# Performance work log

Measured on AMD Instinct MI355X. Metric: run time of the kernel, lower is better.

Reference implementation:

```python
import jax, jax.numpy as jnp
import numpy as np

NUM_INPUT = 700
NUM_HIDDEN = 256
NUM_OUTPUT = 20
WIN = 50
BATCH = 512
DELAYS = (0, 16, 32)
MAX_D = 32
N_LAYERS = 2
THRESH = 0.3
ALPHA = 0.8  # membrane decay tau_m
LENS = 0.5   # surrogate-gradient window

@jax.custom_vjp
def spike_fn(u):
    # Heaviside with rectangular surrogate gradient (ActFun in the torch repo)
    return (u > 0.0).astype(u.dtype)

def _spike_fwd(u):
    return spike_fn(u), u

def _spike_bwd(u, g):
    return (g * (jnp.abs(u) < LENS).astype(u.dtype),)

spike_fn.defvjp(_spike_fwd, _spike_bwd)


def setup_inputs() -> dict:
    key = jax.random.key(0)
    ks = jax.random.split(key, 6)
    def init(k, shape, fan_in):
        return (jax.random.normal(k, shape, jnp.float32) / np.sqrt(fan_in)).astype(jnp.float32)
    return {
        "x":  jax.random.uniform(ks[0], (BATCH, WIN, NUM_INPUT), jnp.float32),
        # one input Linear per delay: [n_delays, H, In]
        "Wd": init(ks[1], (len(DELAYS), NUM_HIDDEN, NUM_INPUT), NUM_INPUT),
        "bd": jnp.zeros((len(DELAYS), NUM_HIDDEN), jnp.float32),
        # per-layer feedforward and recurrent weights
        "Wf": init(ks[2], (N_LAYERS, NUM_HIDDEN, NUM_HIDDEN), NUM_HIDDEN),
        "bf": jnp.zeros((N_LAYERS, NUM_HIDDEN), jnp.float32),
        "Wr": init(ks[3], (N_LAYERS, NUM_HIDDEN, NUM_HIDDEN), NUM_HIDDEN),
        # readout
        "Wo": init(ks[4], (NUM_OUTPUT, NUM_HIDDEN), NUM_HIDDEN),
        "bo": jnp.zeros((NUM_OUTPUT,), jnp.float32),
    }


def _forward(x, Wd, bd, Wf, bf, Wr, Wo, bo):
    B, win, _ = x.shape
    # extended_input: zeros for the first MAX_D steps, then the input
    ext = jnp.pad(x, ((0, 0), (MAX_D, 0), (0, 0)))
    # Precompute summed delayed input currents for all timesteps at once.
    cur = jnp.zeros((B, win, NUM_HIDDEN), x.dtype)
    for i, d in enumerate(DELAYS):
        sl = jax.lax.dynamic_slice_in_dim(ext, MAX_D - d, win, axis=1)
        cur = cur + jnp.einsum('bti,hi->bth', sl, Wd[i]) + bd[i]

    def step(carry, cur_t):
        mems, spks, o_mem, o_spk, o_sum, out_mot = carry
        prev = cur_t  # [B, H] summed delayed-input activations
        new_m, new_s = [], []
        for l in range(N_LAYERS):
            m = mems[l] * ALPHA * (1.0 - spks[l]) + prev @ Wf[l].T + bf[l] + spks[l] @ Wr[l].T
            s = spike_fn(m - THRESH)
            new_m.append(m)
            new_s.append(s)
            prev = s
        o_mem = o_mem * ALPHA * (1.0 - o_spk) + prev @ Wo.T + bo
        o_spk = spike_fn(o_mem - THRESH)
        o_sum = o_sum + o_spk
        out_mot = out_mot + jax.nn.softmax(o_mem, axis=1)
        return (jnp.stack(new_m), jnp.stack(new_s), o_mem, o_spk, o_sum, out_mot), None

    z = jnp.zeros((B, NUM_OUTPUT), x.dtype)
    zh = jnp.zeros((N_LAYERS, B, NUM_HIDDEN), x.dtype)
    carry0 = (zh, zh, z, z, z, z)
    carry, _ = jax.lax.scan(step, carry0, jnp.swapaxes(cur, 0, 1))
    _, _, _, _, o_sum, out_mot = carry
    return (o_sum / win, out_mot)


def reference(x, Wd, bd, Wf, bf, Wr, Wo, bo):
    return _forward(x, Wd, bd, Wf, bf, Wr, Wo, bo)
```

## Files before the change

### kernel.cpp

```cpp
#include <hip/hip_runtime.h>
#include <cstddef>

#define CUR_ELEMS (25600 * 256)
#define WROWS 65792

__global__ __launch_bounds__(256) void k0_transpose(
    const float* __restrict__ Wf, const float* __restrict__ Wr,
    const float* __restrict__ Wo, float* __restrict__ ws) {
  int tid = blockIdx.x * blockDim.x + threadIdx.x;
  float* Wr0T = ws + CUR_ELEMS;
  float* Wf1T = Wr0T + WROWS;
  float* Wr1T = Wf1T + WROWS;
  float* WoT  = Wr1T + WROWS;
  if (tid < WROWS) {
    int k = tid >> 8, h = tid & 255;
    Wr0T[tid] = (k < 256) ? Wr[h * 256 + k] : 0.f;
  } else if (tid < 2 * WROWS) {
    int i = tid - WROWS; int k = i >> 8, h = i & 255;
    Wf1T[i] = (k < 256) ? Wf[65536 + h * 256 + k] : 0.f;
  } else if (tid < 3 * WROWS) {
    int i = tid - 2 * WROWS; int k = i >> 8, h = i & 255;
    Wr1T[i] = (k < 256) ? Wr[65536 + h * 256 + k] : 0.f;
  } else if (tid < 3 * WROWS + 5140) {
    int i = tid - 3 * WROWS; int k = i / 20, j = i - k * 20;
    WoT[i] = (k < 256) ? Wo[j * 256 + k] : 0.f;
  }
}

__global__ __launch_bounds__(256) void k1_cur(
    const float* __restrict__ x, const float* __restrict__ Wd,
    const float* __restrict__ bd, float* __restrict__ cur) {
  __shared__ float As[16][132];
  __shared__ float Bs[16][132];
  const int t  = 49 - blockIdx.y;
  const int bt = blockIdx.x >> 1, ht = blockIdx.x & 1;
  const int b0 = bt * 128, h0 = ht * 128;
  const int tid = threadIdx.x;
  const int tx = tid & 15, ty = tid >> 4;
  const int r = tid & 127, half = tid >> 7;

  float acc[8][8];
#pragma unroll
  for (int i = 0; i < 8; ++i)
#pragma unroll
    for (int j = 0; j < 8; ++j) acc[i][j] = 0.f;

  const int DEL[3] = {0, 16, 32};
#pragma unroll 1
  for (int di = 0; di < 3; ++di) {
    const int d = DEL[di];
    if (t < d) continue;
    const int tsrc = t - d;
    const float* Arow = x + ((size_t)(b0 + r) * 50 + tsrc) * 700;
    const float* Brow = Wd + (size_t)di * 179200 + (size_t)(h0 + r) * 700;
#pragma unroll 1
    for (int k0 = 0; k0 < 700; k0 += 16) {
#pragma unroll
      for (int e = 0; e < 2; ++e) {
        const int kk0 = half * 8 + e * 4;
        float4 av, bv;
        if (k0 + kk0 + 3 < 700) {
          av = *(const float4*)(Arow + k0 + kk0);
          bv = *(const float4*)(Brow + k0 + kk0);
        } else {
          av = make_float4(0.f, 0.f, 0.f, 0.f);
          bv = make_float4(0.f, 0.f, 0.f, 0.f);
        }
        As[kk0 + 0][r] = av.x; As[kk0 + 1][r] = av.y;
        As[kk0 + 2][r] = av.z; As[kk0 + 3][r] = av.w;
        Bs[kk0 + 0][r] = bv.x; Bs[kk0 + 1][r] = bv.y;
        Bs[kk0 + 2][r] = bv.z; Bs[kk0 + 3][r] = bv.w;
      }
      __syncthreads();
#pragma unroll
      for (int kk = 0; kk < 16; ++kk) {
        const float4 a0 = *(const float4*)&As[kk][ty * 4];
        const float4 a1 = *(const float4*)&As[kk][64 + ty * 4];
        const float4 c0 = *(const float4*)&Bs[kk][tx * 4];
        const float4 c1 = *(const float4*)&Bs[kk][64 + tx * 4];
        const float ar[8] = {a0.x, a0.y, a0.z, a0.w, a1.x, a1.y, a1.z, a1.w};
        const float br[8] = {c0.x, c0.y, c0.z, c0.w, c1.x, c1.y, c1.z, c1.w};
#pragma unroll
        for (int rr = 0; rr < 8; ++rr)
#pragma unroll
          for (int cc = 0; cc < 8; ++cc) acc[rr][cc] += ar[rr] * br[cc];
      }
      __syncthreads();
    }
  }
  float bias[8];
#pragma unroll
  for (int q = 0; q < 2; ++q)
#pragma unroll
    for (int c = 0; c < 4; ++c) {
      const int col = h0 + q * 64 + tx * 4 + c;
      bias[q * 4 + c] = bd[col] + bd[256 + col] + bd[512 + col];
    }
#pragma unroll
  for (int p = 0; p < 2; ++p)
#pragma unroll
    for (int rr = 0; rr < 4; ++rr) {
      const int row = b0 + p * 64 + ty * 4 + rr;
      float* dst = cur + ((size_t)t * 512 + row) * 256 + h0;
      const int ai = p * 4 + rr;
      float4 v0 = make_float4(acc[ai][0] + bias[0], acc[ai][1] + bias[1],
                              acc[ai][2] + bias[2], acc[ai][3] + bias[3]);
      float4 v1 = make_float4(acc[ai][4] + bias[4], acc[ai][5] + bias[5],
                              acc[ai][6] + bias[6], acc[ai][7] + bias[7]);
      *(float4*)(dst + tx * 4) = v0;
      *(float4*)(dst + 64 + tx * 4) = v1;
    }
}

__global__ __launch_bounds__(256) void k1b_ff0(
    const float* __restrict__ Wf, const float* __restrict__ bf,
    float* __restrict__ cur) {
  __shared__ float As[16][68];
  __shared__ float Bs[16][260];
  const int m0 = blockIdx.x * 64;
  const int tid = threadIdx.x;
  const int tx = tid & 15, ty = tid >> 4;
  const int lr = tid & 63, akk = (tid >> 6) * 4;

  float acc[4][16];
#pragma unroll
  for (int i = 0; i < 4; ++i)
#pragma unroll
    for (int j = 0; j < 16; ++j) acc[i][j] = 0.f;

#pragma unroll 1
  for (int k0 = 0; k0 < 256; k0 += 16) {
    float4 av = *(const float4*)(cur + (size_t)(m0 + lr) * 256 + k0 + akk);
    As[akk + 0][lr] = av.x; As[akk + 1][lr] = av.y;
    As[akk + 2][lr] = av.z; As[akk + 3][lr] = av.w;
#pragma unroll
    for (int e = 0; e < 4; ++e) {
      const int hh = e * 64 + lr;
      float4 bv = *(const float4*)(Wf + (size_t)hh * 256 + k0 + akk);
      Bs[akk + 0][hh] = bv.x; Bs[akk + 1][hh] = bv.y;
      Bs[akk + 2][hh] = bv.z; Bs[akk + 3][hh] = bv.w;
    }
    __syncthreads();
#pragma unroll
    for (int kk = 0; kk < 16; ++kk) {
      const float4 a = *(const float4*)&As[kk][ty * 4];
      const float ar[4] = {a.x, a.y, a.z, a.w};
#pragma unroll
      for (int q = 0; q < 4; ++q) {
        const float4 bq = *(const float4*)&Bs[kk][q * 64 + tx * 4];
        const float br[4] = {bq.x, bq.y, bq.z, bq.w};
#pragma unroll
        for (int rr = 0; rr < 4; ++rr)
#pragma unroll
          for (int cc = 0; cc < 4; ++cc)
            acc[rr][q * 4 + cc] += ar[rr] * br[cc];
      }
    }
    __syncthreads();
  }
  float bias[16];
#pragma unroll
  for (int q = 0; q < 4; ++q)
#pragma unroll
    for (int c = 0; c < 4; ++c) bias[q * 4 + c] = bf[q * 64 + tx * 4 + c];
#pragma unroll
  for (int rr = 0; rr < 4; ++rr) {
    float* dst = cur + (size_t)(m0 + ty * 4 + rr) * 256;
#pragma unroll
    for (int q = 0; q < 4; ++q) {
      float4 v = make_float4(acc[rr][q * 4 + 0] + bias[q * 4 + 0],
                             acc[rr][q * 4 + 1] + bias[q * 4 + 1],
                             acc[rr][q * 4 + 2] + bias[q * 4 + 2],
                             acc[rr][q * 4 + 3] + bias[q * 4 + 3]);
      *(float4*)(dst + q * 64 + tx * 4) = v;
    }
  }
}

__device__ __forceinline__ float sum16v(const float* w) {
  float s0 = 0.f, s1 = 0.f, s2 = 0.f, s3 = 0.f;
#pragma unroll
  for (int u = 0; u < 16; u += 4) {
    s0 += w[u]; s1 += w[u + 1]; s2 += w[u + 2]; s3 += w[u + 3];
  }
  return (s0 + s1) + (s2 + s3);
}

__device__ __forceinline__ void fetch16(
    const float* __restrict__ baseA, const int* LA_, int nA_,
    const float* __restrict__ baseB, const int* LB_, int g16, int h, float* w) {
  const float* base = (g16 < nA_) ? baseA : baseB;
  const int*   L    = (g16 < nA_) ? LA_ : LB_;
  const int    off  = (g16 < nA_) ? g16 : (g16 - nA_);
#pragma unroll
  for (int q = 0; q < 4; ++q) {
    const int4 l4 = *(const int4*)(L + off + 4 * q);
    w[4 * q + 0] = base[l4.x + h];
    w[4 * q + 1] = base[l4.y + h];
    w[4 * q + 2] = base[l4.z + h];
    w[4 * q + 3] = base[l4.w + h];
  }
}

__device__ __forceinline__ float gather_sum(
    const float* __restrict__ baseA, const int* LA_, int nA_,
    const float* __restrict__ baseB, const int* LB_, int nB_, int h) {
  const int G = (nA_ + nB_) >> 4;
  if (G == 0) return 0.f;
  float acc = 0.f;
  float w0[16], w1[16];
  fetch16(baseA, LA_, nA_, baseB, LB_, 0, h, w0);
  int g = 1;
  for (; g + 2 <= G; g += 2) {
    fetch16(baseA, LA_, nA_, baseB, LB_, g << 4, h, w1);
    acc += sum16v(w0);
    fetch16(baseA, LA_, nA_, baseB, LB_, (g + 1) << 4, h, w0);
    acc += sum16v(w1);
  }
  if (g < G) {
    fetch16(baseA, LA_, nA_, baseB, LB_, g << 4, h, w1);
    acc += sum16v(w0);
    acc += sum16v(w1);
  } else {
    acc += sum16v(w0);
  }
  return acc;
}

__global__ __launch_bounds__(256) void k2_scan(
    const float* __restrict__ ff0, const float* __restrict__ Wr0T,
    const float* __restrict__ Wf1T, const float* __restrict__ Wr1T,
    const float* __restrict__ WoT, const float* __restrict__ bf,
    const float* __restrict__ bo, float* __restrict__ out) {
  __shared__ float spk0[256], spk1[256];
  __shared__ __align__(16) int LC0[272], LC1[272];
  __shared__ int n0_s, n1_s;
  __shared__ float obuf[20];
  const int b = blockIdx.x;
  const int h = threadIdx.x;

  float m0 = 0.f, m1 = 0.f, s0self = 0.f, s1self = 0.f;
  const float bf1v = bf[256 + h];
  const int rl = h - 64;
  const int ro = (rl >= 0) ? rl / 3 : 0;
  const int rc = (rl >= 0) ? rl - ro * 3 : 0;
  float omem = 0.f, ospk = 0.f, osum = 0.f, omot = 0.f;
  const float bov = (rl >= 0 && rl < 20) ? bo[rl] : 0.f;

  if (h == 0) { n0_s = 0; n1_s = 0; }
  __syncthreads();

  const float* ffp = ff0 + (size_t)b * 256 + h;
  for (int t = 0; t < 50; ++t) {
    float acc0 = ffp[(size_t)t * (512 * 256)];
    acc0 += gather_sum(Wr0T, LC0, n0_s, Wr0T, LC0, 0, h);
    m0 = m0 * 0.8f * (1.f - s0self) + acc0;
    s0self = (m0 - 0.3f > 0.f) ? 1.f : 0.f;
    spk0[h] = s0self;
    __syncthreads();
    if (h < 64) {
      int base = 0;
#pragma unroll
      for (int c = 0; c < 4; ++c) {
        const int k = c * 64 + h;
        const bool sp = spk0[k] > 0.f;
        const unsigned long long mk = __ballot(sp);
        const int pos = base + (int)__popcll(mk & ((1ull << h) - 1ull));
        if (sp) LC0[pos] = k << 8;
        base += (int)__popcll(mk);
      }
      const int pad = (-base) & 15;
      if (h < pad) LC0[base + h] = 256 << 8;
      if (h == 0) n0_s = base + pad;
    }
    __syncthreads();
    float acc1 = bf1v + gather_sum(Wf1T, LC0, n0_s, Wr1T, LC1, n1_s, h);
    m1 = m1 * 0.8f * (1.f - s1self) + acc1;
    s1self = (m1 - 0.3f > 0.f) ? 1.f : 0.f;
    spk1[h] = s1self;
    __syncthreads();
    if (h < 64) {
      int base = 0;
#pragma unroll
      for (int c = 0; c < 4; ++c) {
        const int k = c * 64 + h;
        const bool sp = spk1[k] > 0.f;
        const unsigned long long mk = __ballot(sp);
        const int pos = base + (int)__popcll(mk & ((1ull << h) - 1ull));
        if (sp) LC1[pos] = k << 8;
        base += (int)__popcll(mk);
      }
      const int pad = (-base) & 15;
      if (h < pad) LC1[base + h] = 256 << 8;
      if (h == 0) n1_s = base + pad;
    } else if (h < 128) {
      float v = 0.f;
      if (rl < 60) {
        int k = rc;
#pragma unroll 1
        for (int gq = 0; gq < 10; ++gq) {
          float sv[8], wv[8];
#pragma unroll
          for (int u = 0; u < 8; ++u) {
            sv[u] = spk1[k + 3 * u];
            wv[u] = WoT[(k + 3 * u) * 20 + ro];
          }
          float p0 = sv[0] * wv[0], p1 = sv[1] * wv[1];
          float p2 = sv[2] * wv[2], p3 = sv[3] * wv[3];
          p0 += sv[4] * wv[4]; p1 += sv[5] * wv[5];
          p2 += sv[6] * wv[6]; p3 += sv[7] * wv[7];
          v += (p0 + p1) + (p2 + p3);
          k += 24;
        }
        for (; k < 256; k += 3) v += spk1[k] * WoT[k * 20 + ro];
      }
      const float v1 = __shfl_down(v, 1);
      const float v2 = __shfl_down(v, 2);
      v += v1 + v2;
      if (rc == 0 && rl < 60) obuf[ro] = v;
      if (rl >= 0 && rl < 20) {
        const float oacc = bov + obuf[rl];
        omem = omem * 0.8f * (1.f - ospk) + oacc;
        ospk = (omem - 0.3f > 0.f) ? 1.f : 0.f;
        osum += ospk;
        obuf[rl] = omem;
      }
      if (rl >= 0 && rl < 20) {
        float mx = obuf[0];
        for (int j = 1; j < 20; ++j) mx = fmaxf(mx, obuf[j]);
        float sm = 0.f;
        for (int j = 0; j < 20; ++j) sm += expf(obuf[j] - mx);
        omot += expf(omem - mx) / sm;
      }
    }
  }
  if (h >= 64 && h < 84) {
    out[b * 20 + rl] = osum / 50.0f;
    out[10240 + b * 20 + rl] = omot;
  }
}

extern "C" void kernel_launch(void* const* d_in, const int* in_sizes, int n_in,
                              void* d_out, int out_size, void* d_ws, size_t ws_size,
                              hipStream_t stream) {
  const float* x  = (const float*)d_in[0];
  const float* Wd = (const float*)d_in[1];
  const float* bd = (const float*)d_in[2];
  const float* Wf = (const float*)d_in[3];
  const float* bf = (const float*)d_in[4];
  const float* Wr = (const float*)d_in[5];
  const float* Wo = (const float*)d_in[6];
  const float* bo = (const float*)d_in[7];
  float* out = (float*)d_out;
  float* ws  = (float*)d_ws;

  float* cur  = ws;
  float* Wr0T = ws + CUR_ELEMS;
  float* Wf1T = Wr0T + WROWS;
  float* Wr1T = Wf1T + WROWS;
  float* WoT  = Wr1T + WROWS;

  hipLaunchKernelGGL(k0_transpose, dim3(792), dim3(256), 0, stream, Wf, Wr, Wo, ws);
  hipLaunchKernelGGL(k1_cur, dim3(8, 50), dim3(256), 0, stream, x, Wd, bd, cur);
  hipLaunchKernelGGL(k1b_ff0, dim3(400), dim3(256), 0, stream, Wf, bf, cur);
  hipLaunchKernelGGL(k2_scan, dim3(512), dim3(256), 0, stream, cur, Wr0T, Wf1T,
                     Wr1T, WoT, bf, bo, out);
}
```

Baseline: 1.043 ms.

## Run recurrent scan with one wavefront per batch row and register-prefetch GEMM tiles

The scan kernel now uses a single 64-lane wavefront per batch element, with each lane owning four hidden units as float4. Sparse spike lists are built with ballots inside the wavefront, which removes the block-wide __syncthreads between phases, and weight rows are gathered with float4 loads. The output layer now also gathers only the spiking rows of Wo through a third index list. The input GEMM kernel separately prefetches the next K-chunk into registers while computing on the current shared tile. Costs: fewer threads per block and lower occupancy in the scan kernel, and extra register pressure from the prefetch buffers.

```diff
diff --git a/kernel.cpp b/kernel.cpp
--- a/kernel.cpp
+++ b/kernel.cpp
@@ -38,6 +38,7 @@
   const int tid = threadIdx.x;
   const int tx = tid & 15, ty = tid >> 4;
   const int r = tid & 127, half = tid >> 7;
+  const int kk0a = half * 8;
 
   float acc[8][8];
 #pragma unroll
@@ -53,25 +54,36 @@
     const int tsrc = t - d;
     const float* Arow = x + ((size_t)(b0 + r) * 50 + tsrc) * 700;
     const float* Brow = Wd + (size_t)di * 179200 + (size_t)(h0 + r) * 700;
+    float4 pa0, pa1, pb0, pb1;
+    {
+      pa0 = *(const float4*)(Arow + kk0a);
+      pa1 = *(const float4*)(Arow + kk0a + 4);
+      pb0 = *(const float4*)(Brow + kk0a);
+      pb1 = *(const float4*)(Brow + kk0a + 4);
+    }
 #pragma unroll 1
-    for (int k0 = 0; k0 < 700; k0 += 16) {
-#pragma unroll
-      for (int e = 0; e < 2; ++e) {
-        const int kk0 = half * 8 + e * 4;
-        float4 av, bv;
-        if (k0 + kk0 + 3 < 700) {
-          av = *(const float4*)(Arow + k0 + kk0);
-          bv = *(const float4*)(Brow + k0 + kk0);
-        } else {
-          av = make_float4(0.f, 0.f, 0.f, 0.f);
-          bv = make_float4(0.f, 0.f, 0.f, 0.f);
-        }
-        As[kk0 + 0][r] = av.x; As[kk0 + 1][r] = av.y;
-        As[kk0 + 2][r] = av.z; As[kk0 + 3][r] = av.w;
-        Bs[kk0 + 0][r] = bv.x; Bs[kk0 + 1][r] = bv.y;
-        Bs[kk0 + 2][r] = bv.z; Bs[kk0 + 3][r] = bv.w;
+    for (int c = 0; c < 44; ++c) {
+      __syncthreads();
+      As[kk0a + 0][r] = pa0.x; As[kk0a + 1][r] = pa0.y;
+      As[kk0a + 2][r] = pa0.z; As[kk0a + 3][r] = pa0.w;
+      As[kk0a + 4][r] = pa1.x; As[kk0a + 5][r] = pa1.y;
+      As[kk0a + 6][r] = pa1.z; As[kk0a + 7][r] = pa1.w;
+      Bs[kk0a + 0][r] = pb0.x; Bs[kk0a + 1][r] = pb0.y;
+      Bs[kk0a + 2][r] = pb0.z; Bs[kk0a + 3][r] = pb0.w;
+      Bs[kk0a + 4][r] = pb1.x; Bs[kk0a + 5][r] = pb1.y;
+      Bs[kk0a + 6][r] = pb1.z; Bs[kk0a + 7][r] = pb1.w;
+      __syncthreads();
+      if (c + 1 < 44) {
+        const int i0 = (c + 1) * 16 + kk0a, i1 = i0 + 4;
+        pa0 = (i0 < 700) ? *(const float4*)(Arow + i0)
+                         : make_float4(0.f, 0.f, 0.f, 0.f);
+        pa1 = (i1 < 700) ? *(const float4*)(Arow + i1)
+                         : make_float4(0.f, 0.f, 0.f, 0.f);
+        pb0 = (i0 < 700) ? *(const float4*)(Brow + i0)
+                         : make_float4(0.f, 0.f, 0.f, 0.f);
+        pb1 = (i1 < 700) ? *(const float4*)(Brow + i1)
+                         : make_float4(0.f, 0.f, 0.f, 0.f);
       }
-      __syncthreads();
 #pragma unroll
       for (int kk = 0; kk < 16; ++kk) {
         const float4 a0 = *(const float4*)&As[kk][ty * 4];
@@ -85,7 +97,6 @@
 #pragma unroll
           for (int cc = 0; cc < 8; ++cc) acc[rr][cc] += ar[rr] * br[cc];
       }
-      __syncthreads();
     }
   }
   float bias[8];
@@ -177,166 +188,201 @@
   }
 }
 
-__device__ __forceinline__ float sum16v(const float* w) {
-  float s0 = 0.f, s1 = 0.f, s2 = 0.f, s3 = 0.f;
-#pragma unroll
-  for (int u = 0; u < 16; u += 4) {
-    s0 += w[u]; s1 += w[u + 1]; s2 += w[u + 2]; s3 += w[u + 3];
-  }
-  return (s0 + s1) + (s2 + s3);
-}
-
-__device__ __forceinline__ void fetch16(
-    const float* __restrict__ baseA, const int* LA_, int nA_,
-    const float* __restrict__ baseB, const int* LB_, int g16, int h, float* w) {
-  const float* base = (g16 < nA_) ? baseA : baseB;
-  const int*   L    = (g16 < nA_) ? LA_ : LB_;
-  const int    off  = (g16 < nA_) ? g16 : (g16 - nA_);
-#pragma unroll
-  for (int q = 0; q < 4; ++q) {
-    const int4 l4 = *(const int4*)(L + off + 4 * q);
-    w[4 * q + 0] = base[l4.x + h];
-    w[4 * q + 1] = base[l4.y + h];
-    w[4 * q + 2] = base[l4.z + h];
-    w[4 * q + 3] = base[l4.w + h];
-  }
-}
-
-__device__ __forceinline__ float gather_sum(
-    const float* __restrict__ baseA, const int* LA_, int nA_,
-    const float* __restrict__ baseB, const int* LB_, int nB_, int h) {
-  const int G = (nA_ + nB_) >> 4;
-  if (G == 0) return 0.f;
-  float acc = 0.f;
-  float w0[16], w1[16];
-  fetch16(baseA, LA_, nA_, baseB, LB_, 0, h, w0);
+__device__ __forceinline__ void load8rows(const float* __restrict__ W,
+                                          const int* LC, int j, int l4,
+                                          float4* w) {
+  const int4 a = *(const int4*)(LC + j);
+  const int4 c = *(const int4*)(LC + j + 4);
+  w[0] = *(const float4*)(W + a.x + l4);
+  w[1] = *(const float4*)(W + a.y + l4);
+  w[2] = *(const float4*)(W + a.z + l4);
+  w[3] = *(const float4*)(W + a.w + l4);
+  w[4] = *(const float4*)(W + c.x + l4);
+  w[5] = *(const float4*)(W + c.y + l4);
+  w[6] = *(const float4*)(W + c.z + l4);
+  w[7] = *(const float4*)(W + c.w + l4);
+}
+
+__device__ __forceinline__ void add8rows(float4& acc, const float4* w) {
+  float4 t0, t1, t2, t3;
+  t0.x = w[0].x + w[1].x; t0.y = w[0].y + w[1].y; t0.z = w[0].z + w[1].z; t0.w = w[0].w + w[1].w;
+  t1.x = w[2].x + w[3].x; t1.y = w[2].y + w[3].y; t1.z = w[2].z + w[3].z; t1.w = w[2].w + w[3].w;
+  t2.x = w[4].x + w[5].x; t2.y = w[4].y + w[5].y; t2.z = w[4].z + w[5].z; t2.w = w[4].w + w[5].w;
+  t3.x = w[6].x + w[7].x; t3.y = w[6].y + w[7].y; t3.z = w[6].z + w[7].z; t3.w = w[6].w + w[7].w;
+  t0.x += t1.x; t0.y += t1.y; t0.z += t1.z; t0.w += t1.w;
+  t2.x += t3.x; t2.y += t3.y; t2.z += t3.z; t2.w += t3.w;
+  acc.x += t0.x + t2.x; acc.y += t0.y + t2.y;
+  acc.z += t0.z + t2.z; acc.w += t0.w + t2.w;
+}
+
+__device__ __forceinline__ float4 gather_rows(const float* __restrict__ W,
+                                              const int* LC, int n, int l4) {
+  float4 acc = make_float4(0.f, 0.f, 0.f, 0.f);
+  const int G = n >> 3;
+  if (G == 0) return acc;
+  float4 wa[8], wb[8];
+  load8rows(W, LC, 0, l4, wa);
   int g = 1;
   for (; g + 2 <= G; g += 2) {
-    fetch16(baseA, LA_, nA_, baseB, LB_, g << 4, h, w1);
-    acc += sum16v(w0);
-    fetch16(baseA, LA_, nA_, baseB, LB_, (g + 1) << 4, h, w0);
-    acc += sum16v(w1);
+    load8rows(W, LC, g * 8, l4, wb);
+    add8rows(acc, wa);
+    load8rows(W, LC, (g + 1) * 8, l4, wa);
+    add8rows(acc, wb);
   }
   if (g < G) {
-    fetch16(baseA, LA_, nA_, baseB, LB_, g << 4, h, w1);
-    acc += sum16v(w0);
-    acc += sum16v(w1);
+    load8rows(W, LC, g * 8, l4, wb);
+    add8rows(acc, wa);
+    add8rows(acc, wb);
   } else {
-    acc += sum16v(w0);
+    add8rows(acc, wa);
   }
   return acc;
 }
 
-__global__ __launch_bounds__(256) void k2_scan(
+__device__ __forceinline__ void load8o(const float* __restrict__ W,
+                                       const int* LCb, int j, int lane,
+                                       float* w) {
+  const int4 a = *(const int4*)(LCb + j);
+  const int4 c = *(const int4*)(LCb + j + 4);
+  w[0] = W[a.x + lane]; w[1] = W[a.y + lane];
+  w[2] = W[a.z + lane]; w[3] = W[a.w + lane];
+  w[4] = W[c.x + lane]; w[5] = W[c.y + lane];
+  w[6] = W[c.z + lane]; w[7] = W[c.w + lane];
+}
+
+__device__ __forceinline__ float add8o(const float* w) {
+  return ((w[0] + w[1]) + (w[2] + w[3])) + ((w[4] + w[5]) + (w[6] + w[7]));
+}
+
+__device__ __forceinline__ float gather_out(const float* __restrict__ W,
+                                            const int* LCb, int n, int lane) {
+  float acc = 0.f;
+  const int G = n >> 3;
+  if (G == 0) return acc;
+  float wa[8], wb[8];
+  load8o(W, LCb, 0, lane, wa);
+  int g = 1;
+  for (; g + 2 <= G; g += 2) {
+    load8o(W, LCb, g * 8, lane, wb);
+    acc += add8o(wa);
+    load8o(W, LCb, (g + 1) * 8, lane, wa);
+    acc += add8o(wb);
+  }
+  if (g < G) {
+    load8o(W, LCb, g * 8, lane, wb);
+    acc += add8o(wa);
+    acc += add8o(wb);
+  } else {
+    acc += add8o(wa);
+  }
+  return acc;
+}
+
+__global__ __launch_bounds__(64) void k2_scan(
     const float* __restrict__ ff0, const float* __restrict__ Wr0T,
     const float* __restrict__ Wf1T, const float* __restrict__ Wr1T,
     const float* __restrict__ WoT, const float* __restrict__ bf,
     const float* __restrict__ bo, float* __restrict__ out) {
-  __shared__ float spk0[256], spk1[256];
-  __shared__ __align__(16) int LC0[272], LC1[272];
-  __shared__ int n0_s, n1_s;
+  __shared__ __align__(16) int LC0[264];
+  __shared__ __align__(16) int LC1[264];
+  __shared__ __align__(16) int LCb[264];
   __shared__ float obuf[20];
   const int b = blockIdx.x;
-  const int h = threadIdx.x;
-
-  float m0 = 0.f, m1 = 0.f, s0self = 0.f, s1self = 0.f;
-  const float bf1v = bf[256 + h];
-  const int rl = h - 64;
-  const int ro = (rl >= 0) ? rl / 3 : 0;
-  const int rc = (rl >= 0) ? rl - ro * 3 : 0;
+  const int lane = threadIdx.x;
+  const int l4 = lane * 4;
+  const unsigned long long lb = (1ull << lane) - 1ull;
+
+  float4 m0 = make_float4(0.f, 0.f, 0.f, 0.f), m1 = m0;
+  float4 s0v = m0, s1v = m0;
+  const float4 bf1v = *(const float4*)(bf + 256 + l4);
   float omem = 0.f, ospk = 0.f, osum = 0.f, omot = 0.f;
-  const float bov = (rl >= 0 && rl < 20) ? bo[rl] : 0.f;
-
-  if (h == 0) { n0_s = 0; n1_s = 0; }
-  __syncthreads();
-
-  const float* ffp = ff0 + (size_t)b * 256 + h;
+  const float bov = (lane < 20) ? bo[lane] : 0.f;
+  int n0 = 0, n1 = 0;
+
+  const float* ffp = ff0 + (size_t)b * 256 + l4;
+  float4 ff = *(const float4*)ffp;
+
+#pragma unroll 1
   for (int t = 0; t < 50; ++t) {
-    float acc0 = ffp[(size_t)t * (512 * 256)];
-    acc0 += gather_sum(Wr0T, LC0, n0_s, Wr0T, LC0, 0, h);
-    m0 = m0 * 0.8f * (1.f - s0self) + acc0;
-    s0self = (m0 - 0.3f > 0.f) ? 1.f : 0.f;
-    spk0[h] = s0self;
-    __syncthreads();
-    if (h < 64) {
+    float4 ffn = ff;
+    if (t < 49) ffn = *(const float4*)(ffp + (size_t)(t + 1) * 131072);
+    {
+      const float4 g = gather_rows(Wr0T, LC0, n0, l4);
+      m0.x = m0.x * 0.8f * (1.f - s0v.x) + ff.x + g.x;
+      m0.y = m0.y * 0.8f * (1.f - s0v.y) + ff.y + g.y;
+      m0.z = m0.z * 0.8f * (1.f - s0v.z) + ff.z + g.z;
+      m0.w = m0.w * 0.8f * (1.f - s0v.w) + ff.w + g.w;
+      s0v.x = (m0.x - 0.3f > 0.f) ? 1.f : 0.f;
+      s0v.y = (m0.y - 0.3f > 0.f) ? 1.f : 0.f;
+      s0v.z = (m0.z - 0.3f > 0.f) ? 1.f : 0.f;
+      s0v.w = (m0.w - 0.3f > 0.f) ? 1.f : 0.f;
+    }
+    {
+      const float sv[4] = {s0v.x, s0v.y, s0v.z, s0v.w};
       int base = 0;
 #pragma unroll
-      for (int c = 0; c < 4; ++c) {
-        const int k = c * 64 + h;
-        const bool sp = spk0[k] > 0.f;
+      for (int q = 0; q < 4; ++q) {
+        const bool sp = sv[q] > 0.f;
         const unsigned long long mk = __ballot(sp);
-        const int pos = base + (int)__popcll(mk & ((1ull << h) - 1ull));
-        if (sp) LC0[pos] = k << 8;
+        const int pos = base + (int)__popcll(mk & lb);
+        if (sp) LC0[pos] = (l4 + q) << 8;
         base += (int)__popcll(mk);
       }
-      const int pad = (-base) & 15;
-      if (h < pad) LC0[base + h] = 256 << 8;
-      if (h == 0) n0_s = base + pad;
-    }
-    __syncthreads();
-    float acc1 = bf1v + gather_sum(Wf1T, LC0, n0_s, Wr1T, LC1, n1_s, h);
-    m1 = m1 * 0.8f * (1.f - s1self) + acc1;
-    s1self = (m1 - 0.3f > 0.f) ? 1.f : 0.f;
-    spk1[h] = s1self;
-    __syncthreads();
-    if (h < 64) {
+      const int pad = (-base) & 7;
+      if (lane < pad) LC0[base + lane] = 256 << 8;
+      n0 = base + pad;
+    }
+    {
+      const float4 g1 = gather_rows(Wf1T, LC0, n0, l4);
+      const float4 g2 = gather_rows(Wr1T, LC1, n1, l4);
+      m1.x = m1.x * 0.8f * (1.f - s1v.x) + bf1v.x + g1.x + g2.x;
+      m1.y = m1.y * 0.8f * (1.f - s1v.y) + bf1v.y + g1.y + g2.y;
+      m1.z = m1.z * 0.8f * (1.f - s1v.z) + bf1v.z + g1.z + g2.z;
+      m1.w = m1.w * 0.8f * (1.f - s1v.w) + bf1v.w + g1.w + g2.w;
+      s1v.x = (m1.x - 0.3f > 0.f) ? 1.f : 0.f;
+      s1v.y = (m1.y - 0.3f > 0.f) ? 1.f : 0.f;
+      s1v.z = (m1.z - 0.3f > 0.f) ? 1.f : 0.f;
+      s1v.w = (m1.w - 0.3f > 0.f) ? 1.f : 0.f;
+    }
+    {
+      const float sv[4] = {s1v.x, s1v.y, s1v.z, s1v.w};
       int base = 0;
 #pragma unroll
-      for (int c = 0; c < 4; ++c) {
-        const int k = c * 64 + h;
-        const bool sp = spk1[k] > 0.f;
+      for (int q = 0; q < 4; ++q) {
+        const bool sp = sv[q] > 0.f;
         const unsigned long long mk = __ballot(sp);
-        const int pos = base + (int)__popcll(mk & ((1ull << h) - 1ull));
-        if (sp) LC1[pos] = k << 8;
+        const int pos = base + (int)__popcll(mk & lb);
+        if (sp) { LC1[pos] = (l4 + q) << 8; LCb[pos] = (l4 + q) * 20; }
         base += (int)__popcll(mk);
       }
-      const int pad = (-base) & 15;
-      if (h < pad) LC1[base + h] = 256 << 8;
-      if (h == 0) n1_s = base + pad;
-    } else if (h < 128) {
-      float v = 0.f;
-      if (rl < 60) {
-        int k = rc;
-#pragma unroll 1
-        for (int gq = 0; gq < 10; ++gq) {
-          float sv[8], wv[8];
-#pragma unroll
-          for (int u = 0; u < 8; ++u) {
-            sv[u] = spk1[k + 3 * u];
-            wv[u] = WoT[(k + 3 * u) * 20 + ro];
-          }
-          float p0 = sv[0] * wv[0], p1 = sv[1] * wv[1];
-          float p2 = sv[2] * wv[2], p3 = sv[3] * wv[3];
-          p0 += sv[4] * wv[4]; p1 += sv[5] * wv[5];
-          p2 += sv[6] * wv[6]; p3 += sv[7] * wv[7];
-          v += (p0 + p1) + (p2 + p3);
-          k += 24;
-        }
-        for (; k < 256; k += 3) v += spk1[k] * WoT[k * 20 + ro];
-      }
-      const float v1 = __shfl_down(v, 1);
-      const float v2 = __shfl_down(v, 2);
-      v += v1 + v2;
-      if (rc == 0 && rl < 60) obuf[ro] = v;
-      if (rl >= 0 && rl < 20) {
-        const float oacc = bov + obuf[rl];
-        omem = omem * 0.8f * (1.f - ospk) + oacc;
-        ospk = (omem - 0.3f > 0.f) ? 1.f : 0.f;
-        osum += ospk;
-        obuf[rl] = omem;
-      }
-      if (rl >= 0 && rl < 20) {
-        float mx = obuf[0];
-        for (int j = 1; j < 20; ++j) mx = fmaxf(mx, obuf[j]);
-        float sm = 0.f;
-        for (int j = 0; j < 20; ++j) sm += expf(obuf[j] - mx);
-        omot += expf(omem - mx) / sm;
-      }
-    }
-  }
-  if (h >= 64 && h < 84) {
-    out[b * 20 + rl] = osum / 50.0f;
-    out[10240 + b * 20 + rl] = omot;
+      const int pad = (-base) & 7;
+      if (lane < pad) { LC1[base + lane] = 256 << 8; LCb[base + lane] = 256 * 20; }
+      n1 = base + pad;
+    }
+    if (lane < 20) {
+      const float v = gather_out(WoT, LCb, n1, lane);
+      omem = omem * 0.8f * (1.f - ospk) + bov + v;
+      ospk = (omem - 0.3f > 0.f) ? 1.f : 0.f;
+      osum += ospk;
+      obuf[lane] = omem;
+    }
+    if (lane < 20) {
+      float ov[20];
+#pragma unroll
+      for (int j = 0; j < 20; ++j) ov[j] = obuf[j];
+      float mx = ov[0];
+#pragma unroll
+      for (int j = 1; j < 20; ++j) mx = fmaxf(mx, ov[j]);
+      float sm = 0.f;
+#pragma unroll
+      for (int j = 0; j < 20; ++j) sm += expf(ov[j] - mx);
+      omot += expf(omem - mx) / sm;
+    }
+    ff = ffn;
+  }
+  if (lane < 20) {
+    out[b * 20 + lane] = osum / 50.0f;
+    out[10240 + b * 20 + lane] = omot;
   }
 }
 
@@ -363,6 +409,6 @@
   hipLaunchKernelGGL(k0_transpose, dim3(792), dim3(256), 0, stream, Wf, Wr, Wo, ws);
   hipLaunchKernelGGL(k1_cur, dim3(8, 50), dim3(256), 0, stream, x, Wd, bd, cur);
   hipLaunchKernelGGL(k1b_ff0, dim3(400), dim3(256), 0, stream, Wf, bf, cur);
-  hipLaunchKernelGGL(k2_scan, dim3(512), dim3(256), 0, stream, cur, Wr0T, Wf1T,
+  hipLaunchKernelGGL(k2_scan, dim3(512), dim3(64), 0, stream, cur, Wr0T, Wf1T,
                      Wr1T, WoT, bf, bo, out);
 }
```

New measurement: 940.6 us. 9.8% less time.
